# Optimization experiments

Measured on AMD Instinct MI355X. Metric: run time of the kernel, lower is better.

## Reference

```python
import jax, jax.numpy as jnp
import numpy as np

N = 50000
E = 800000
IN_C = 128
HID = 64
HEADS = 4
OUT_C = 64


def setup_inputs() -> dict:
    key = jax.random.key(0)
    ks = jax.random.split(key, 20)
    s = 0.05
    inp = {
        "x": jax.random.normal(ks[0], (N, IN_C), dtype=jnp.float32),
        "edge_index": jax.random.randint(ks[1], (2, E), 0, N, dtype=jnp.int64),
        # layer 0: in=128 -> heads=4, C=64
        "W0": jax.random.normal(ks[2], (IN_C, HEADS * HID), jnp.float32) * s,
        "a0s": jax.random.normal(ks[3], (HEADS, HID), jnp.float32) * s,
        "a0d": jax.random.normal(ks[4], (HEADS, HID), jnp.float32) * s,
        "b0": jnp.zeros((HEADS * HID,), jnp.float32),
        # layer 1: 256 -> heads=4, C=64
        "W1": jax.random.normal(ks[5], (HEADS * HID, HEADS * HID), jnp.float32) * s,
        "a1s": jax.random.normal(ks[6], (HEADS, HID), jnp.float32) * s,
        "a1d": jax.random.normal(ks[7], (HEADS, HID), jnp.float32) * s,
        "b1": jnp.zeros((HEADS * HID,), jnp.float32),
        # layer 2: 256 -> heads=1, C=64
        "W2": jax.random.normal(ks[8], (HEADS * HID, HID), jnp.float32) * s,
        "a2s": jax.random.normal(ks[9], (1, HID), jnp.float32) * s,
        "a2d": jax.random.normal(ks[10], (1, HID), jnp.float32) * s,
        "b2": jnp.zeros((HID,), jnp.float32),
        # prediction head: Linear(64 -> 64)
        "hw": jax.random.normal(ks[11], (HID, OUT_C), jnp.float32) * s,
        "hb": jnp.zeros((OUT_C,), jnp.float32),
    }
    return inp


def gat_conv(x, src, dst, W, a_s, a_d, b, heads, n_nodes):
    # x: [N, F_in]; returns [N, heads*C]
    C = a_s.shape[1]
    h = (x @ W).reshape(n_nodes, heads, C)          # [N,H,C]
    alpha_s = jnp.sum(h * a_s, axis=-1)             # [N,H]
    alpha_d = jnp.sum(h * a_d, axis=-1)             # [N,H]
    e = jax.nn.leaky_relu(alpha_s[src] + alpha_d[dst], negative_slope=0.2)  # [E,H]
    m = jax.ops.segment_max(e, dst, num_segments=n_nodes)                  # per-dst max
    ex = jnp.exp(e - m[dst])
    denom = jax.ops.segment_sum(ex, dst, num_segments=n_nodes)
    alpha = ex / (denom[dst] + 1e-16)               # [E,H]
    out = jax.ops.segment_sum(alpha[:, :, None] * h[src], dst, num_segments=n_nodes)
    return out.reshape(n_nodes, heads * C) + b


def reference(x, edge_index, W0, a0s, a0d, b0, W1, a1s, a1d, b1, W2, a2s, a2d, b2, hw, hb):
    n = x.shape[0]
    # PyG GATConv default add_self_loops=True
    loop = jnp.arange(n, dtype=edge_index.dtype)
    src = jnp.concatenate([edge_index[0], loop])
    dst = jnp.concatenate([edge_index[1], loop])

    h = gat_conv(x, src, dst, W0, a0s, a0d, b0, HEADS, n)
    h = jax.nn.relu(h)
    h = gat_conv(h, src, dst, W1, a1s, a1d, b1, HEADS, n)
    h = jax.nn.relu(h)
    h = gat_conv(h, src, dst, W2, a2s, a2d, b2, 1, n)
    # batch is None -> mean over all nodes, keepdim
    g = jnp.mean(h, axis=0, keepdims=True)          # [1, HID]
    return g @ hw + hb                               # [1, OUT_C]
```

## Files before the change

kernel.cpp:

```cpp
#include <hip/hip_runtime.h>
#include <hip/hip_bf16.h>
#include <cstddef>

#define NN 50000
#define EE 800000
#define NB ((NN + 255) / 256)

typedef __attribute__((ext_vector_type(8))) short short8;
typedef __attribute__((ext_vector_type(4))) float f32x4;

#define GLB __attribute__((address_space(1)))
#define LDS __attribute__((address_space(3)))

__device__ __forceinline__ float leaky(float x) { return x >= 0.f ? x : 0.2f * x; }
__device__ __forceinline__ float bf2f(unsigned short u) {
  return __uint_as_float(((unsigned int)u) << 16);
}
__device__ __forceinline__ float bflo(unsigned int v) { return __uint_as_float(v << 16); }
__device__ __forceinline__ float bfhi(unsigned int v) { return __uint_as_float(v & 0xFFFF0000u); }
__device__ __forceinline__ unsigned short f2bf(float f) {
  __hip_bfloat16 b = __float2bfloat16(f);
  return __builtin_bit_cast(unsigned short, b);
}
__device__ __forceinline__ void accum8(float a, uint4 v, float* acc) {
  acc[0] += a * bflo(v.x); acc[1] += a * bfhi(v.x);
  acc[2] += a * bflo(v.y); acc[3] += a * bfhi(v.y);
  acc[4] += a * bflo(v.z); acc[5] += a * bfhi(v.z);
  acc[6] += a * bflo(v.w); acc[7] += a * bfhi(v.w);
}

__global__ __launch_bounds__(256) void gemm256_k(const unsigned short* __restrict__ A,
                                                 const unsigned short* __restrict__ Bt,
                                                 unsigned short* __restrict__ Cb,
                                                 int K,
                                                 const float* __restrict__ a_s,
                                                 const float* __restrict__ a_d,
                                                 float* __restrict__ als,
                                                 float* __restrict__ ald,
                                                 float* __restrict__ selfex) {
  __shared__ __align__(16) unsigned short As[2][64 * 32];
  __shared__ __align__(16) unsigned short Bs[2][256 * 32];
  const int tid = threadIdx.x;
  const int lane = tid & 63;
  const int w = tid >> 6;
  const int bm = blockIdx.x * 64;
  const int quad = lane >> 4;
  const int l16 = lane & 15;
  const int lrow = lane >> 2;
  const int lseg = lane & 3;
  f32x4 acc[16] = {};
  const int nk = K >> 5;

  auto stage = [&](int buf, int kc) {
    {
      int row = w * 16 + lrow;
      int g = lseg ^ ((row >> 2) & 3);
      int sr = bm + row; if (sr >= NN) sr = NN - 1;
      const unsigned short* gp = A + (size_t)sr * K + kc + g * 8;
      __builtin_amdgcn_global_load_lds((const GLB void*)gp,
                                       (LDS void*)&As[buf][(w * 16) * 32], 16, 0, 0);
    }
#pragma unroll
    for (int c = 0; c < 4; ++c) {
      int row = w * 64 + c * 16 + lrow;
      int g = lseg ^ ((row >> 2) & 3);
      const unsigned short* gp = Bt + (size_t)row * K + kc + g * 8;
      __builtin_amdgcn_global_load_lds((const GLB void*)gp,
                                       (LDS void*)&Bs[buf][(w * 64 + c * 16) * 32], 16, 0, 0);
    }
  };

  stage(0, 0);
  __syncthreads();
  for (int t = 0; t < nk; ++t) {
    const int cur = t & 1;
    if (t + 1 < nk) stage(cur ^ 1, (t + 1) * 32);
    const int ra = w * 16 + l16;
    short8 afr = *(const short8*)&As[cur][ra * 32 + ((quad ^ ((ra >> 2) & 3)) << 3)];
#pragma unroll
    for (int nt = 0; nt < 16; ++nt) {
      int rb = nt * 16 + l16;
      short8 bfr = *(const short8*)&Bs[cur][rb * 32 + ((quad ^ ((rb >> 2) & 3)) << 3)];
      acc[nt] = __builtin_amdgcn_mfma_f32_16x16x32_bf16(afr, bfr, acc[nt], 0, 0, 0);
    }
    __syncthreads();
  }
  float vs[4][4] = {};
  float vd[4][4] = {};
#pragma unroll
  for (int nt = 0; nt < 16; ++nt) {
    const int h = nt >> 2;
    const float asv = a_s[h * 64 + (nt & 3) * 16 + l16];
    const float adv = a_d[h * 64 + (nt & 3) * 16 + l16];
#pragma unroll
    for (int reg = 0; reg < 4; ++reg) {
      unsigned short c = f2bf(acc[nt][reg]);
      int r = bm + w * 16 + quad * 4 + reg;
      if (r < NN) Cb[(size_t)r * 256 + nt * 16 + l16] = c;
      float hv = bf2f(c);
      vs[h][reg] += hv * asv;
      vd[h][reg] += hv * adv;
    }
  }
#pragma unroll
  for (int off = 1; off < 16; off <<= 1) {
#pragma unroll
    for (int h = 0; h < 4; ++h)
#pragma unroll
      for (int reg = 0; reg < 4; ++reg) {
        vs[h][reg] += __shfl_xor(vs[h][reg], off, 64);
        vd[h][reg] += __shfl_xor(vd[h][reg], off, 64);
      }
  }
  if (l16 == 0) {
#pragma unroll
    for (int reg = 0; reg < 4; ++reg) {
      int r = bm + w * 16 + quad * 4 + reg;
      if (r < NN) {
        float4 fs = make_float4(vs[0][reg], vs[1][reg], vs[2][reg], vs[3][reg]);
        float4 fd = make_float4(vd[0][reg], vd[1][reg], vd[2][reg], vd[3][reg]);
        *(float4*)&als[(size_t)r * 4] = fs;
        *(float4*)&ald[(size_t)r * 4] = fd;
        float4 se = make_float4(__expf(leaky(fs.x + fd.x)), __expf(leaky(fs.y + fd.y)),
                                __expf(leaky(fs.z + fd.z)), __expf(leaky(fs.w + fd.w)));
        *(float4*)&selfex[(size_t)r * 4] = se;
      }
    }
  }
}

__global__ __launch_bounds__(256) void gemm64_k(const unsigned short* __restrict__ A,
                                                const unsigned short* __restrict__ Bt,
                                                unsigned short* __restrict__ Cb,
                                                int K,
                                                const float* __restrict__ a_s,
                                                const float* __restrict__ a_d,
                                                float* __restrict__ als,
                                                float* __restrict__ ald,
                                                float* __restrict__ selfex) {
  __shared__ __align__(16) unsigned short As[2][64 * 32];
  __shared__ __align__(16) unsigned short Bs[2][64 * 32];
  const int tid = threadIdx.x;
  const int lane = tid & 63;
  const int w = tid >> 6;
  const int bm = blockIdx.x * 64;
  const int quad = lane >> 4;
  const int l16 = lane & 15;
  const int lrow = lane >> 2;
  const int lseg = lane & 3;
  f32x4 acc[4] = {};
  const int nk = K >> 5;

  auto stage = [&](int buf, int kc) {
    {
      int row = w * 16 + lrow;
      int g = lseg ^ ((row >> 2) & 3);
      int sr = bm + row; if (sr >= NN) sr = NN - 1;
      const unsigned short* gp = A + (size_t)sr * K + kc + g * 8;
      __builtin_amdgcn_global_load_lds((const GLB void*)gp,
                                       (LDS void*)&As[buf][(w * 16) * 32], 16, 0, 0);
    }
    {
      int row = w * 16 + lrow;
      int g = lseg ^ ((row >> 2) & 3);
      const unsigned short* gp = Bt + (size_t)row * K + kc + g * 8;
      __builtin_amdgcn_global_load_lds((const GLB void*)gp,
                                       (LDS void*)&Bs[buf][(w * 16) * 32], 16, 0, 0);
    }
  };

  stage(0, 0);
  __syncthreads();
  for (int t = 0; t < nk; ++t) {
    const int cur = t & 1;
    if (t + 1 < nk) stage(cur ^ 1, (t + 1) * 32);
    const int ra = w * 16 + l16;
    short8 afr = *(const short8*)&As[cur][ra * 32 + ((quad ^ ((ra >> 2) & 3)) << 3)];
#pragma unroll
    for (int nt = 0; nt < 4; ++nt) {
      int rb = nt * 16 + l16;
      short8 bfr = *(const short8*)&Bs[cur][rb * 32 + ((quad ^ ((rb >> 2) & 3)) << 3)];
      acc[nt] = __builtin_amdgcn_mfma_f32_16x16x32_bf16(afr, bfr, acc[nt], 0, 0, 0);
    }
    __syncthreads();
  }
  float vs[4] = {};
  float vd[4] = {};
#pragma unroll
  for (int nt = 0; nt < 4; ++nt) {
    const float asv = a_s[nt * 16 + l16];
    const float adv = a_d[nt * 16 + l16];
#pragma unroll
    for (int reg = 0; reg < 4; ++reg) {
      unsigned short c = f2bf(acc[nt][reg]);
      int r = bm + w * 16 + quad * 4 + reg;
      if (r < NN) Cb[(size_t)r * 64 + nt * 16 + l16] = c;
      float hv = bf2f(c);
      vs[reg] += hv * asv;
      vd[reg] += hv * adv;
    }
  }
#pragma unroll
  for (int off = 1; off < 16; off <<= 1) {
#pragma unroll
    for (int reg = 0; reg < 4; ++reg) {
      vs[reg] += __shfl_xor(vs[reg], off, 64);
      vd[reg] += __shfl_xor(vd[reg], off, 64);
    }
  }
  if (l16 == 0) {
#pragma unroll
    for (int reg = 0; reg < 4; ++reg) {
      int r = bm + w * 16 + quad * 4 + reg;
      if (r < NN) {
        als[r] = vs[reg];
        ald[r] = vd[reg];
        selfex[r] = __expf(leaky(vs[reg] + vd[reg]));
      }
    }
  }
}

__global__ __launch_bounds__(256) void hist_k(const int* __restrict__ ei, int* deg) {
  int i = blockIdx.x * 256 + threadIdx.x;
  if (i < EE) atomicAdd(&deg[ei[EE + i]], 1);
}

__global__ __launch_bounds__(256) void scan1_k(const int* __restrict__ deg,
                                               int* __restrict__ incl,
                                               int* __restrict__ partial) {
  __shared__ int s[256];
  int t = threadIdx.x;
  int i = blockIdx.x * 256 + t;
  int v = (i < NN) ? deg[i] : 0;
  s[t] = v;
  __syncthreads();
  for (int off = 1; off < 256; off <<= 1) {
    int u = (t >= off) ? s[t - off] : 0;
    __syncthreads();
    s[t] += u;
    __syncthreads();
  }
  if (i < NN) incl[i] = s[t];
  if (t == 255) partial[blockIdx.x] = s[255];
}

__global__ __launch_bounds__(256) void scan23_k(const int* __restrict__ deg,
                                                const int* __restrict__ incl,
                                                const int* __restrict__ partial,
                                                int* __restrict__ rowptr,
                                                int* __restrict__ cursor) {
  __shared__ int s[256];
  __shared__ int ex[256];
  int t = threadIdx.x;
  int v = (t < NB) ? partial[t] : 0;
  s[t] = v;
  __syncthreads();
  for (int off = 1; off < 256; off <<= 1) {
    int u = (t >= off) ? s[t - off] : 0;
    __syncthreads();
    s[t] += u;
    __syncthreads();
  }
  ex[t] = s[t] - v;
  __syncthreads();
  int base = ex[blockIdx.x];
  int i = blockIdx.x * 256 + t;
  if (i < NN) {
    int r = base + incl[i] - deg[i];
    rowptr[i] = r;
    cursor[i] = r;
  }
}

__global__ __launch_bounds__(256) void scatter_k(const int* __restrict__ ei,
                                                 int* __restrict__ cursor,
                                                 int* __restrict__ csr_src) {
  int i = blockIdx.x * 256 + threadIdx.x;
  if (i >= EE) return;
  int d = ei[EE + i];
  int p = atomicAdd(&cursor[d], 1);
  csr_src[p] = ei[i];
}

__global__ __launch_bounds__(256) void aggr4c_k(const int* __restrict__ rowptr,
                                                const int* __restrict__ deg,
                                                const int* __restrict__ csr_src,
                                                const float* __restrict__ als,
                                                const float* __restrict__ ald,
                                                const float* __restrict__ selfex,
                                                const uint4* __restrict__ hb4,
                                                const float* __restrict__ bias,
                                                uint4* __restrict__ out4) {
  const int dst = blockIdx.x * 4 + (threadIdx.x >> 6);
  const int lane = threadIdx.x & 63;
  const int slot = lane >> 4;
  const int l16 = lane & 15;
  const int head = l16 >> 2;
  const int rs = rowptr[dst];
  const int dg = deg[dst];
  const float aldv = ald[dst * 4 + head];

  float acc[16] = {};
  float dsum = 0.f;
  if (slot == 0) {
    float a = selfex[dst * 4 + head];
    dsum += a;
    uint4 v0 = hb4[(size_t)dst * 32 + l16 * 2];
    uint4 v1 = hb4[(size_t)dst * 32 + l16 * 2 + 1];
    accum8(a, v0, acc);
    accum8(a, v1, acc + 8);
  }
  int j = slot;
  for (; j + 4 < dg; j += 8) {
    int s0 = csr_src[rs + j];
    int s1 = csr_src[rs + j + 4];
    float e0 = als[s0 * 4 + head];
    float e1 = als[s1 * 4 + head];
    uint4 va0 = hb4[(size_t)s0 * 32 + l16 * 2];
    uint4 vb0 = hb4[(size_t)s0 * 32 + l16 * 2 + 1];
    uint4 va1 = hb4[(size_t)s1 * 32 + l16 * 2];
    uint4 vb1 = hb4[(size_t)s1 * 32 + l16 * 2 + 1];
    float a0 = __expf(leaky(e0 + aldv));
    float a1 = __expf(leaky(e1 + aldv));
    dsum += a0 + a1;
    accum8(a0, va0, acc);
    accum8(a0, vb0, acc + 8);
    accum8(a1, va1, acc);
    accum8(a1, vb1, acc + 8);
  }
  for (; j < dg; j += 4) {
    int s0 = csr_src[rs + j];
    float e0 = als[s0 * 4 + head];
    uint4 va0 = hb4[(size_t)s0 * 32 + l16 * 2];
    uint4 vb0 = hb4[(size_t)s0 * 32 + l16 * 2 + 1];
    float a0 = __expf(leaky(e0 + aldv));
    dsum += a0;
    accum8(a0, va0, acc);
    accum8(a0, vb0, acc + 8);
  }
#pragma unroll
  for (int k = 0; k < 16; ++k) {
    acc[k] += __shfl_xor(acc[k], 16, 64);
    acc[k] += __shfl_xor(acc[k], 32, 64);
  }
  dsum += __shfl_xor(dsum, 16, 64);
  dsum += __shfl_xor(dsum, 32, 64);
  if (slot == 0) {
    const float inv = 1.f / (dsum + 1e-16f);
    const float* bz = bias + l16 * 16;
    uint4 o0, o1;
    float c0, c1;
    c0 = fmaxf(acc[0] * inv + bz[0], 0.f);   c1 = fmaxf(acc[1] * inv + bz[1], 0.f);
    o0.x = ((unsigned int)f2bf(c1) << 16) | f2bf(c0);
    c0 = fmaxf(acc[2] * inv + bz[2], 0.f);   c1 = fmaxf(acc[3] * inv + bz[3], 0.f);
    o0.y = ((unsigned int)f2bf(c1) << 16) | f2bf(c0);
    c0 = fmaxf(acc[4] * inv + bz[4], 0.f);   c1 = fmaxf(acc[5] * inv + bz[5], 0.f);
    o0.z = ((unsigned int)f2bf(c1) << 16) | f2bf(c0);
    c0 = fmaxf(acc[6] * inv + bz[6], 0.f);   c1 = fmaxf(acc[7] * inv + bz[7], 0.f);
    o0.w = ((unsigned int)f2bf(c1) << 16) | f2bf(c0);
    c0 = fmaxf(acc[8] * inv + bz[8], 0.f);   c1 = fmaxf(acc[9] * inv + bz[9], 0.f);
    o1.x = ((unsigned int)f2bf(c1) << 16) | f2bf(c0);
    c0 = fmaxf(acc[10] * inv + bz[10], 0.f); c1 = fmaxf(acc[11] * inv + bz[11], 0.f);
    o1.y = ((unsigned int)f2bf(c1) << 16) | f2bf(c0);
    c0 = fmaxf(acc[12] * inv + bz[12], 0.f); c1 = fmaxf(acc[13] * inv + bz[13], 0.f);
    o1.z = ((unsigned int)f2bf(c1) << 16) | f2bf(c0);
    c0 = fmaxf(acc[14] * inv + bz[14], 0.f); c1 = fmaxf(acc[15] * inv + bz[15], 0.f);
    o1.w = ((unsigned int)f2bf(c1) << 16) | f2bf(c0);
    out4[(size_t)dst * 32 + l16 * 2] = o0;
    out4[(size_t)dst * 32 + l16 * 2 + 1] = o1;
  }
}

__global__ __launch_bounds__(256) void aggr1c_k(const int* __restrict__ rowptr,
                                                const int* __restrict__ deg,
                                                const int* __restrict__ csr_src,
                                                const float* __restrict__ als,
                                                const float* __restrict__ ald,
                                                const float* __restrict__ selfex,
                                                const uint4* __restrict__ hb4,
                                                const float* __restrict__ bias,
                                                float* __restrict__ out) {
  const int dst = blockIdx.x * 4 + (threadIdx.x >> 6);
  const int lane = threadIdx.x & 63;
  const int slot = lane >> 3;
  const int c8 = lane & 7;
  const int rs = rowptr[dst];
  const int dg = deg[dst];
  const float aldv = ald[dst];

  float acc[8] = {};
  float dsum = 0.f;
  if (slot == 0) {
    float a = selfex[dst];
    dsum += a;
    uint4 v = hb4[(size_t)dst * 8 + c8];
    accum8(a, v, acc);
  }
  for (int j = slot; j < dg; j += 8) {
    int s = csr_src[rs + j];
    float e = als[s];
    uint4 v = hb4[(size_t)s * 8 + c8];
    float a = __expf(leaky(e + aldv));
    dsum += a;
    accum8(a, v, acc);
  }
#pragma unroll
  for (int k = 0; k < 8; ++k) {
    acc[k] += __shfl_xor(acc[k], 8, 64);
    acc[k] += __shfl_xor(acc[k], 16, 64);
    acc[k] += __shfl_xor(acc[k], 32, 64);
  }
  dsum += __shfl_xor(dsum, 8, 64);
  dsum += __shfl_xor(dsum, 16, 64);
  dsum += __shfl_xor(dsum, 32, 64);
  if (slot == 0) {
    const float inv = 1.f / (dsum + 1e-16f);
    const float4 bz0 = *(const float4*)(bias + c8 * 8);
    const float4 bz1 = *(const float4*)(bias + c8 * 8 + 4);
    float4 o0 = make_float4(acc[0] * inv + bz0.x, acc[1] * inv + bz0.y,
                            acc[2] * inv + bz0.z, acc[3] * inv + bz0.w);
    float4 o1 = make_float4(acc[4] * inv + bz1.x, acc[5] * inv + bz1.y,
                            acc[6] * inv + bz1.z, acc[7] * inv + bz1.w);
    *(float4*)(out + (size_t)dst * 64 + c8 * 8) = o0;
    *(float4*)(out + (size_t)dst * 64 + c8 * 8 + 4) = o1;
  }
}

__global__ __launch_bounds__(256) void prep_k(const float2* __restrict__ x2,
                                              unsigned int* __restrict__ xb_u,
                                              const float* __restrict__ W0,
                                              unsigned short* __restrict__ W0t,
                                              const float* __restrict__ W1,
                                              unsigned short* __restrict__ W1t,
                                              const float* __restrict__ W2,
                                              unsigned short* __restrict__ W2t,
                                              int* __restrict__ deg,
                                              float* __restrict__ g) {
  int bid = blockIdx.x;
  int tid = threadIdx.x;
  if (bid < 12500) {
    int i = bid * 256 + tid;
    float2 v = x2[i];
    xb_u[i] = ((unsigned int)f2bf(v.y) << 16) | f2bf(v.x);
    return;
  }
  if (bid < 12948) {
    int r = (bid - 12500) * 256 + tid;
    if (r < 32768) {
      int n = r >> 7, k = r & 127;
      W0t[n * 128 + k] = f2bf(W0[k * 256 + n]);
    } else if (r < 98304) {
      int rr = r - 32768;
      int n = rr >> 8, k = rr & 255;
      W1t[n * 256 + k] = f2bf(W1[k * 256 + n]);
    } else {
      int rr = r - 98304;
      int n = rr >> 8, k = rr & 255;
      W2t[n * 256 + k] = f2bf(W2[k * 64 + n]);
    }
    return;
  }
  if (bid < 13144) {
    int i = (bid - 12948) * 256 + tid;
    if (i < NN) deg[i] = 0;
    return;
  }
  if (tid < 68) g[tid] = 0.f;
}

__global__ __launch_bounds__(256) void colsum_head_k(const float* __restrict__ h2,
                                                     float* __restrict__ g,
                                                     unsigned int* __restrict__ cnt,
                                                     const float* __restrict__ hw,
                                                     const float* __restrict__ hb,
                                                     float* __restrict__ out) {
  __shared__ float s[256];
  __shared__ float sg[64];
  __shared__ unsigned int sdone;
  int tid = threadIdx.x;
  int c = tid & 63, rg = tid >> 6;
  float acc = 0.f;
  for (int n = blockIdx.x * 4 + rg; n < NN; n += gridDim.x * 4)
    acc += h2[n * 64 + c];
  s[tid] = acc;
  __syncthreads();
  if (tid < 64) atomicAdd(&g[c], s[c] + s[64 + c] + s[128 + c] + s[192 + c]);
  __threadfence();
  __syncthreads();
  if (tid == 0) sdone = atomicAdd(cnt, 1);
  __syncthreads();
  if (sdone != gridDim.x - 1) return;
  if (tid < 64) sg[tid] = atomicAdd(&g[tid], 0.f);
  __syncthreads();
  if (tid < 64) {
    const float invN = 1.0f / (float)NN;
    float a2 = hb[tid];
#pragma unroll 8
    for (int cc = 0; cc < 64; ++cc) a2 += sg[cc] * invN * hw[cc * 64 + tid];
    out[tid] = a2;
  }
}

extern "C" void kernel_launch(void* const* d_in, const int* in_sizes, int n_in,
                              void* d_out, int out_size, void* d_ws, size_t ws_size,
                              hipStream_t stream) {
  const float* x   = (const float*)d_in[0];
  const int*   ei  = (const int*)d_in[1];
  const float* W0  = (const float*)d_in[2];
  const float* a0s = (const float*)d_in[3];
  const float* a0d = (const float*)d_in[4];
  const float* b0  = (const float*)d_in[5];
  const float* W1  = (const float*)d_in[6];
  const float* a1s = (const float*)d_in[7];
  const float* a1d = (const float*)d_in[8];
  const float* b1  = (const float*)d_in[9];
  const float* W2  = (const float*)d_in[10];
  const float* a2s = (const float*)d_in[11];
  const float* a2d = (const float*)d_in[12];
  const float* b2  = (const float*)d_in[13];
  const float* hw  = (const float*)d_in[14];
  const float* hb  = (const float*)d_in[15];
  float* out = (float*)d_out;

  char* w = (char*)d_ws;
  unsigned short* xb   = (unsigned short*)w; w += (size_t)NN * 128 * 2;
  unsigned short* bufG = (unsigned short*)w; w += (size_t)NN * 256 * 2;
  unsigned short* bufA = (unsigned short*)w; w += (size_t)NN * 256 * 2;
  float* bufF = (float*)w;                   w += (size_t)NN * 64 * 4;
  unsigned short* W0t = (unsigned short*)w;  w += 256 * 128 * 2;
  unsigned short* W1t = (unsigned short*)w;  w += 256 * 256 * 2;
  unsigned short* W2t = (unsigned short*)w;  w += 64 * 256 * 2;
  float* als  = (float*)w;    w += (size_t)NN * 4 * 4;
  float* ald  = (float*)w;    w += (size_t)NN * 4 * 4;
  float* sfx  = (float*)w;    w += (size_t)NN * 4 * 4;
  int* deg     = (int*)w;     w += (size_t)NN * 4;
  int* rowptr  = (int*)w;     w += (size_t)NN * 4;
  int* cursor  = (int*)w;     w += (size_t)NN * 4;
  int* incl    = (int*)w;     w += (size_t)NN * 4;
  int* partial = (int*)w;     w += 256 * 4;
  int* csr_src = (int*)w;     w += (size_t)EE * 4;
  float* g    = (float*)w;    w += 256;

  prep_k<<<13145, 256, 0, stream>>>((const float2*)x, (unsigned int*)xb,
                                    W0, W0t, W1, W1t, W2, W2t, deg, g);

  hist_k<<<(EE + 255) / 256, 256, 0, stream>>>(ei, deg);
  scan1_k<<<NB, 256, 0, stream>>>(deg, incl, partial);
  scan23_k<<<NB, 256, 0, stream>>>(deg, incl, partial, rowptr, cursor);
  scatter_k<<<(EE + 255) / 256, 256, 0, stream>>>(ei, cursor, csr_src);

  const int G64 = (NN + 63) / 64;
  const int GA = NN / 4;

  auto layer4 = [&](const unsigned short* in, int K, const unsigned short* Wt,
                    const float* a_s, const float* a_d, const float* bias,
                    unsigned short* hbuf, unsigned short* obuf) {
    gemm256_k<<<G64, 256, 0, stream>>>(in, Wt, hbuf, K, a_s, a_d, als, ald, sfx);
    aggr4c_k<<<GA, 256, 0, stream>>>(rowptr, deg, csr_src, als, ald, sfx,
                                     (const uint4*)hbuf, bias, (uint4*)obuf);
  };

  layer4(xb, 128, W0t, a0s, a0d, b0, bufG, bufA);
  layer4(bufA, 256, W1t, a1s, a1d, b1, bufG, bufA);

  gemm64_k<<<G64, 256, 0, stream>>>(bufA, W2t, bufG, 256, a2s, a2d, als, ald, sfx);
  aggr1c_k<<<GA, 256, 0, stream>>>(rowptr, deg, csr_src, als, ald, sfx,
                                   (const uint4*)bufG, b2, bufF);

  colsum_head_k<<<256, 256, 0, stream>>>(bufF, g, (unsigned int*)(g + 64), hw, hb, out);
}
```

Before: 444.3 us.

## Split 256-wide GEMM over two column blocks and stage K in 128-wide chunks

```diff
diff --git a/kernel.cpp b/kernel.cpp
--- a/kernel.cpp
+++ b/kernel.cpp
@@ -29,7 +29,7 @@
   acc[6] += a * bflo(v.w); acc[7] += a * bfhi(v.w);
 }
 
-__global__ __launch_bounds__(256) void gemm256_k(const unsigned short* __restrict__ A,
+__global__ __launch_bounds__(256) void gemm128_k(const unsigned short* __restrict__ A,
                                                  const unsigned short* __restrict__ Bt,
                                                  unsigned short* __restrict__ Cb,
                                                  int K,
@@ -38,65 +38,67 @@
                                                  float* __restrict__ als,
                                                  float* __restrict__ ald,
                                                  float* __restrict__ selfex) {
-  __shared__ __align__(16) unsigned short As[2][64 * 32];
-  __shared__ __align__(16) unsigned short Bs[2][256 * 32];
+  __shared__ __align__(16) unsigned short As[4][64 * 32];
+  __shared__ __align__(16) unsigned short Bs[4][128 * 32];
   const int tid = threadIdx.x;
   const int lane = tid & 63;
   const int w = tid >> 6;
   const int bm = blockIdx.x * 64;
+  const int bn = blockIdx.y * 128;
   const int quad = lane >> 4;
   const int l16 = lane & 15;
   const int lrow = lane >> 2;
   const int lseg = lane & 3;
-  f32x4 acc[16] = {};
-  const int nk = K >> 5;
-
-  auto stage = [&](int buf, int kc) {
-    {
-      int row = w * 16 + lrow;
-      int g = lseg ^ ((row >> 2) & 3);
-      int sr = bm + row; if (sr >= NN) sr = NN - 1;
-      const unsigned short* gp = A + (size_t)sr * K + kc + g * 8;
-      __builtin_amdgcn_global_load_lds((const GLB void*)gp,
-                                       (LDS void*)&As[buf][(w * 16) * 32], 16, 0, 0);
-    }
-#pragma unroll
-    for (int c = 0; c < 4; ++c) {
-      int row = w * 64 + c * 16 + lrow;
-      int g = lseg ^ ((row >> 2) & 3);
-      const unsigned short* gp = Bt + (size_t)row * K + kc + g * 8;
-      __builtin_amdgcn_global_load_lds((const GLB void*)gp,
-                                       (LDS void*)&Bs[buf][(w * 64 + c * 16) * 32], 16, 0, 0);
-    }
-  };
-
-  stage(0, 0);
-  __syncthreads();
-  for (int t = 0; t < nk; ++t) {
-    const int cur = t & 1;
-    if (t + 1 < nk) stage(cur ^ 1, (t + 1) * 32);
-    const int ra = w * 16 + l16;
-    short8 afr = *(const short8*)&As[cur][ra * 32 + ((quad ^ ((ra >> 2) & 3)) << 3)];
-#pragma unroll
-    for (int nt = 0; nt < 16; ++nt) {
-      int rb = nt * 16 + l16;
-      short8 bfr = *(const short8*)&Bs[cur][rb * 32 + ((quad ^ ((rb >> 2) & 3)) << 3)];
-      acc[nt] = __builtin_amdgcn_mfma_f32_16x16x32_bf16(afr, bfr, acc[nt], 0, 0, 0);
+  f32x4 acc[8] = {};
+
+  for (int kv = 0; kv < K; kv += 128) {
+    if (kv) __syncthreads();
+#pragma unroll
+    for (int ks = 0; ks < 4; ++ks) {
+      const int kc = kv + ks * 32;
+      {
+        int row = w * 16 + lrow;
+        int g = lseg ^ ((row >> 2) & 3);
+        int sr = bm + row; if (sr >= NN) sr = NN - 1;
+        const unsigned short* gp = A + (size_t)sr * K + kc + g * 8;
+        __builtin_amdgcn_global_load_lds((const GLB void*)gp,
+                                         (LDS void*)&As[ks][(w * 16) * 32], 16, 0, 0);
+      }
+#pragma unroll
+      for (int c = 0; c < 2; ++c) {
+        int row = w * 32 + c * 16 + lrow;
+        int g = lseg ^ ((row >> 2) & 3);
+        const unsigned short* gp = Bt + (size_t)(bn + row) * K + kc + g * 8;
+        __builtin_amdgcn_global_load_lds((const GLB void*)gp,
+                                         (LDS void*)&Bs[ks][(w * 32 + c * 16) * 32], 16, 0, 0);
+      }
     }
     __syncthreads();
-  }
-  float vs[4][4] = {};
-  float vd[4][4] = {};
-#pragma unroll
-  for (int nt = 0; nt < 16; ++nt) {
+#pragma unroll
+    for (int ks = 0; ks < 4; ++ks) {
+      const int ra = w * 16 + l16;
+      short8 afr = *(const short8*)&As[ks][ra * 32 + ((quad ^ ((ra >> 2) & 3)) << 3)];
+#pragma unroll
+      for (int nt = 0; nt < 8; ++nt) {
+        int rb = nt * 16 + l16;
+        short8 bfr = *(const short8*)&Bs[ks][rb * 32 + ((quad ^ ((rb >> 2) & 3)) << 3)];
+        acc[nt] = __builtin_amdgcn_mfma_f32_16x16x32_bf16(afr, bfr, acc[nt], 0, 0, 0);
+      }
+    }
+  }
+  const int h0 = blockIdx.y * 2;
+  float vs[2][4] = {};
+  float vd[2][4] = {};
+#pragma unroll
+  for (int nt = 0; nt < 8; ++nt) {
     const int h = nt >> 2;
-    const float asv = a_s[h * 64 + (nt & 3) * 16 + l16];
-    const float adv = a_d[h * 64 + (nt & 3) * 16 + l16];
+    const float asv = a_s[(h0 + h) * 64 + (nt & 3) * 16 + l16];
+    const float adv = a_d[(h0 + h) * 64 + (nt & 3) * 16 + l16];
 #pragma unroll
     for (int reg = 0; reg < 4; ++reg) {
       unsigned short c = f2bf(acc[nt][reg]);
       int r = bm + w * 16 + quad * 4 + reg;
-      if (r < NN) Cb[(size_t)r * 256 + nt * 16 + l16] = c;
+      if (r < NN) Cb[(size_t)r * 256 + bn + nt * 16 + l16] = c;
       float hv = bf2f(c);
       vs[h][reg] += hv * asv;
       vd[h][reg] += hv * adv;
@@ -105,7 +107,7 @@
 #pragma unroll
   for (int off = 1; off < 16; off <<= 1) {
 #pragma unroll
-    for (int h = 0; h < 4; ++h)
+    for (int h = 0; h < 2; ++h)
 #pragma unroll
       for (int reg = 0; reg < 4; ++reg) {
         vs[h][reg] += __shfl_xor(vs[h][reg], off, 64);
@@ -117,29 +119,28 @@
     for (int reg = 0; reg < 4; ++reg) {
       int r = bm + w * 16 + quad * 4 + reg;
       if (r < NN) {
-        float4 fs = make_float4(vs[0][reg], vs[1][reg], vs[2][reg], vs[3][reg]);
-        float4 fd = make_float4(vd[0][reg], vd[1][reg], vd[2][reg], vd[3][reg]);
-        *(float4*)&als[(size_t)r * 4] = fs;
-        *(float4*)&ald[(size_t)r * 4] = fd;
-        float4 se = make_float4(__expf(leaky(fs.x + fd.x)), __expf(leaky(fs.y + fd.y)),
-                                __expf(leaky(fs.z + fd.z)), __expf(leaky(fs.w + fd.w)));
-        *(float4*)&selfex[(size_t)r * 4] = se;
-      }
-    }
-  }
-}
-
-__global__ __launch_bounds__(256) void gemm64_k(const unsigned short* __restrict__ A,
-                                                const unsigned short* __restrict__ Bt,
-                                                unsigned short* __restrict__ Cb,
-                                                int K,
-                                                const float* __restrict__ a_s,
-                                                const float* __restrict__ a_d,
-                                                float* __restrict__ als,
-                                                float* __restrict__ ald,
-                                                float* __restrict__ selfex) {
-  __shared__ __align__(16) unsigned short As[2][64 * 32];
-  __shared__ __align__(16) unsigned short Bs[2][64 * 32];
+#pragma unroll
+        for (int h = 0; h < 2; ++h) {
+          als[(size_t)r * 4 + h0 + h] = vs[h][reg];
+          ald[(size_t)r * 4 + h0 + h] = vd[h][reg];
+          selfex[(size_t)r * 4 + h0 + h] = __expf(leaky(vs[h][reg] + vd[h][reg]));
+        }
+      }
+    }
+  }
+}
+
+__global__ __launch_bounds__(256) void gemm64v_k(const unsigned short* __restrict__ A,
+                                                 const unsigned short* __restrict__ Bt,
+                                                 unsigned short* __restrict__ Cb,
+                                                 int K,
+                                                 const float* __restrict__ a_s,
+                                                 const float* __restrict__ a_d,
+                                                 float* __restrict__ als,
+                                                 float* __restrict__ ald,
+                                                 float* __restrict__ selfex) {
+  __shared__ __align__(16) unsigned short As[4][64 * 32];
+  __shared__ __align__(16) unsigned short Bs[4][64 * 32];
   const int tid = threadIdx.x;
   const int lane = tid & 63;
   const int w = tid >> 6;
@@ -149,40 +150,40 @@
   const int lrow = lane >> 2;
   const int lseg = lane & 3;
   f32x4 acc[4] = {};
-  const int nk = K >> 5;
-
-  auto stage = [&](int buf, int kc) {
-    {
-      int row = w * 16 + lrow;
-      int g = lseg ^ ((row >> 2) & 3);
-      int sr = bm + row; if (sr >= NN) sr = NN - 1;
-      const unsigned short* gp = A + (size_t)sr * K + kc + g * 8;
-      __builtin_amdgcn_global_load_lds((const GLB void*)gp,
-                                       (LDS void*)&As[buf][(w * 16) * 32], 16, 0, 0);
-    }
-    {
-      int row = w * 16 + lrow;
-      int g = lseg ^ ((row >> 2) & 3);
-      const unsigned short* gp = Bt + (size_t)row * K + kc + g * 8;
-      __builtin_amdgcn_global_load_lds((const GLB void*)gp,
-                                       (LDS void*)&Bs[buf][(w * 16) * 32], 16, 0, 0);
-    }
-  };
-
-  stage(0, 0);
-  __syncthreads();
-  for (int t = 0; t < nk; ++t) {
-    const int cur = t & 1;
-    if (t + 1 < nk) stage(cur ^ 1, (t + 1) * 32);
-    const int ra = w * 16 + l16;
-    short8 afr = *(const short8*)&As[cur][ra * 32 + ((quad ^ ((ra >> 2) & 3)) << 3)];
-#pragma unroll
-    for (int nt = 0; nt < 4; ++nt) {
-      int rb = nt * 16 + l16;
-      short8 bfr = *(const short8*)&Bs[cur][rb * 32 + ((quad ^ ((rb >> 2) & 3)) << 3)];
-      acc[nt] = __builtin_amdgcn_mfma_f32_16x16x32_bf16(afr, bfr, acc[nt], 0, 0, 0);
+
+  for (int kv = 0; kv < K; kv += 128) {
+    if (kv) __syncthreads();
+#pragma unroll
+    for (int ks = 0; ks < 4; ++ks) {
+      const int kc = kv + ks * 32;
+      {
+        int row = w * 16 + lrow;
+        int g = lseg ^ ((row >> 2) & 3);
+        int sr = bm + row; if (sr >= NN) sr = NN - 1;
+        const unsigned short* gp = A + (size_t)sr * K + kc + g * 8;
+        __builtin_amdgcn_global_load_lds((const GLB void*)gp,
+                                         (LDS void*)&As[ks][(w * 16) * 32], 16, 0, 0);
+      }
+      {
+        int row = w * 16 + lrow;
+        int g = lseg ^ ((row >> 2) & 3);
+        const unsigned short* gp = Bt + (size_t)row * K + kc + g * 8;
+        __builtin_amdgcn_global_load_lds((const GLB void*)gp,
+                                         (LDS void*)&Bs[ks][(w * 16) * 32], 16, 0, 0);
+      }
     }
     __syncthreads();
+#pragma unroll
+    for (int ks = 0; ks < 4; ++ks) {
+      const int ra = w * 16 + l16;
+      short8 afr = *(const short8*)&As[ks][ra * 32 + ((quad ^ ((ra >> 2) & 3)) << 3)];
+#pragma unroll
+      for (int nt = 0; nt < 4; ++nt) {
+        int rb = nt * 16 + l16;
+        short8 bfr = *(const short8*)&Bs[ks][rb * 32 + ((quad ^ ((rb >> 2) & 3)) << 3)];
+        acc[nt] = __builtin_amdgcn_mfma_f32_16x16x32_bf16(afr, bfr, acc[nt], 0, 0, 0);
+      }
+    }
   }
   float vs[4] = {};
   float vd[4] = {};
@@ -556,7 +557,7 @@
   auto layer4 = [&](const unsigned short* in, int K, const unsigned short* Wt,
                     const float* a_s, const float* a_d, const float* bias,
                     unsigned short* hbuf, unsigned short* obuf) {
-    gemm256_k<<<G64, 256, 0, stream>>>(in, Wt, hbuf, K, a_s, a_d, als, ald, sfx);
+    gemm128_k<<<dim3(G64, 2), 256, 0, stream>>>(in, Wt, hbuf, K, a_s, a_d, als, ald, sfx);
     aggr4c_k<<<GA, 256, 0, stream>>>(rowptr, deg, csr_src, als, ald, sfx,
                                      (const uint4*)hbuf, bias, (uint4*)obuf);
   };
@@ -564,7 +565,7 @@
   layer4(xb, 128, W0t, a0s, a0d, b0, bufG, bufA);
   layer4(bufA, 256, W1t, a1s, a1d, b1, bufG, bufA);
 
-  gemm64_k<<<G64, 256, 0, stream>>>(bufA, W2t, bufG, 256, a2s, a2d, als, ald, sfx);
+  gemm64v_k<<<G64, 256, 0, stream>>>(bufA, W2t, bufG, 256, a2s, a2d, als, ald, sfx);
   aggr1c_k<<<GA, 256, 0, stream>>>(rowptr, deg, csr_src, als, ald, sfx,
                                    (const uint4*)bufG, b2, bufF);
 
```

Measured after the change: 431.6 us. 2.8% less time.
